# Kernel tuning notes

Measured on AMD Instinct MI355X. Metric: run time of the kernel, lower is better.

The kernel has to match this reference:

```python
import jax, jax.numpy as jnp
import numpy as np

N_NODES = 100000
N_EDGES = 3200000
N_GRAPHS = 128
HIDDEN = 128
DEPTH = 3


def setup_inputs() -> dict:
    key = jax.random.key(0)
    ks = jax.random.split(key, 12)
    x = jax.random.normal(ks[0], (N_NODES, 1), dtype=jnp.float32)
    edge_index = jax.random.randint(ks[1], (2, N_EDGES), 0, N_NODES, dtype=jnp.int64)
    batch = jnp.sort(jax.random.randint(ks[2], (N_NODES,), 0, N_GRAPHS, dtype=jnp.int64))
    s = 1.0 / np.sqrt(HIDDEN)
    return {
        "x": x,
        "edge_index": edge_index,
        "batch": batch,
        "W_emb": jax.random.normal(ks[3], (1, HIDDEN), dtype=jnp.float32),
        "b_emb": jax.random.normal(ks[4], (HIDDEN,), dtype=jnp.float32) * 0.01,
        "W_gnn": jax.random.normal(ks[5], (DEPTH, HIDDEN, HIDDEN), dtype=jnp.float32) * s,
        "b_gnn": jax.random.normal(ks[6], (DEPTH, HIDDEN), dtype=jnp.float32) * 0.01,
        "W_c1": jax.random.normal(ks[7], (HIDDEN, HIDDEN // 2), dtype=jnp.float32) * s,
        "b_c1": jax.random.normal(ks[8], (HIDDEN // 2,), dtype=jnp.float32) * 0.01,
        "W_c2": jax.random.normal(ks[9], (HIDDEN // 2, 1), dtype=jnp.float32) * s,
        "b_c2": jax.random.normal(ks[10], (1,), dtype=jnp.float32) * 0.01,
    }


def reference(x, edge_index, batch, W_emb, b_emb, W_gnn, b_gnn, W_c1, b_c1, W_c2, b_c2):
    # --- GCN normalization (self-loops + symmetric deg^-1/2) ---
    loop = jnp.arange(N_NODES, dtype=edge_index.dtype)
    row = jnp.concatenate([edge_index[0], loop])  # source nodes
    col = jnp.concatenate([edge_index[1], loop])  # target nodes
    deg = jax.ops.segment_sum(jnp.ones_like(col, dtype=jnp.float32), col, num_segments=N_NODES)
    dinv = jnp.where(deg > 0, jax.lax.rsqrt(jnp.maximum(deg, 1.0)), 0.0)
    norm = dinv[row] * dinv[col]  # [E+N]

    # --- node embedding ---
    h = x @ W_emb + b_emb  # [N, H]

    # --- GCN layers: linear -> gather -> normalize -> scatter-add -> bias -> relu ---
    for l in range(DEPTH):
        h_lin = h @ W_gnn[l]                       # [N, H]
        msgs = h_lin[row] * norm[:, None]          # [E+N, H]
        agg = jax.ops.segment_sum(msgs, col, num_segments=N_NODES)
        h = jax.nn.relu(agg + b_gnn[l])

    # --- global mean pool per graph ---
    counts = jax.ops.segment_sum(jnp.ones((N_NODES,), jnp.float32), batch, num_segments=N_GRAPHS)
    sums = jax.ops.segment_sum(h, batch, num_segments=N_GRAPHS)
    g = sums / jnp.maximum(counts, 1.0)[:, None]   # [G, H]

    # --- classifier (dropout is identity in eval) ---
    z = jax.nn.relu(g @ W_c1 + b_c1)
    out = jax.nn.sigmoid(z @ W_c2 + b_c2)          # [G, 1]
    return out.squeeze(-1)                          # [G]
```

## Files before the change

kernel.cpp:

```cpp
#include <hip/hip_runtime.h>
#include <math.h>

#define HID 128
#define CAP 96
#define TILE 8192
#define WSH 9
#define BUKCAP 24576

typedef unsigned int uint;
typedef unsigned short ushort;
typedef float f32x2 __attribute__((ext_vector_type(2)));
typedef float f32x4 __attribute__((ext_vector_type(4)));
typedef short bf16x8 __attribute__((ext_vector_type(8)));

__device__ inline ushort f2bf(float f) {
    uint u = __float_as_uint(f);
    return (ushort)((u + 0x7fffu + ((u >> 16) & 1u)) >> 16);
}
__device__ inline uint packbf(float a, float b) {
    return (uint)f2bf(a) | ((uint)f2bf(b) << 16);
}

__device__ inline f32x2 fp8lo(uint q) { return __builtin_amdgcn_cvt_pk_f32_fp8(q, false); }
__device__ inline f32x2 fp8hi(uint q) { return __builtin_amdgcn_cvt_pk_f32_fp8(q, true); }
__device__ inline uint pack4fp8(float a, float b, float c, float d) {
    int t = __builtin_amdgcn_cvt_pk_fp8_f32(a, b, 0, false);
    return (uint)__builtin_amdgcn_cvt_pk_fp8_f32(c, d, t, true);
}
__device__ inline long long as_i64(uint2 u) {
    union { uint2 a; long long b; } c;
    c.a = u;
    return c.b;
}


__global__ void __launch_bounds__(256) k_part(const int* __restrict__ row,
                                              const int* __restrict__ col,
                                              int* __restrict__ bukCur,
                                              uint* __restrict__ recs, int E) {
    __shared__ int hist[256];
    __shared__ int hist2[256];
    __shared__ uint base[256];
    int t = threadIdx.x;
    hist[t] = 0;
    hist2[t] = 0;
    __syncthreads();
    int i0 = blockIdx.x * TILE;
    int i1 = min(E, i0 + TILE);
    for (int i = i0 + t; i < i1; i += 256) {
        int b = col[i] >> WSH;
        atomicAdd(&hist[b], 1);
    }
    __syncthreads();
    if (hist[t] > 0) base[t] = (uint)atomicAdd(&bukCur[t], hist[t]);
    __syncthreads();
    for (int i = i0 + t; i < i1; i += 256) {
        int c = col[i];
        int b = c >> WSH;
        uint p = (uint)atomicAdd(&hist2[b], 1);
        uint idx = base[b] + p;
        if (idx < BUKCAP)
            recs[(size_t)b * BUKCAP + idx] = (uint)row[i] | ((uint)(c & 511) << 17);
    }
}

__global__ void __launch_bounds__(256) k_fbin(const uint* __restrict__ recs,
                                              const int* __restrict__ bukCur,
                                              const float* __restrict__ x,
                                              int* __restrict__ cnt,
                                              int* __restrict__ ebin,
                                              float* __restrict__ dinv,
                                              float2* __restrict__ pk0, int N) {
    __shared__ int lcnt[512];
    int b = blockIdx.x;
    int t = threadIdx.x;
    lcnt[t] = 0;
    lcnt[t + 256] = 0;
    __syncthreads();
    int n = min(bukCur[b], BUKCAP);
    const uint* rp = recs + (size_t)b * BUKCAP;
    int cbase = b << WSH;
    for (int j = t; j < n; j += 256) {
        uint u = rp[j];
        int r = (int)(u & 0x1FFFFu);
        int cl = (int)(u >> 17);
        int p = atomicAdd(&lcnt[cl], 1);
        if (p < CAP) ebin[(size_t)(cbase + cl) * CAP + p] = r << 5;
    }
    __syncthreads();
    int c0 = cbase + t;
    if (c0 < N) {
        cnt[c0] = lcnt[t];
        float d = rsqrtf((float)lcnt[t] + 1.0f);
        dinv[c0] = d;
        pk0[c0] = make_float2(d, d * x[c0]);
    }
    int c1 = cbase + t + 256;
    if (c1 < N) {
        cnt[c1] = lcnt[t + 256];
        float d = rsqrtf((float)lcnt[t + 256] + 1.0f);
        dinv[c1] = d;
        pk0[c1] = make_float2(d, d * x[c1]);
    }
}


__global__ void k_wprep(const float* __restrict__ W_emb, const float* __restrict__ b_emb,
                        const float* __restrict__ W_gnn,
                        float* __restrict__ u, float* __restrict__ v,
                        uint2* __restrict__ wfrag) {
    int b = blockIdx.x;
    int t = threadIdx.x;
    if (b < 16) {
        int gid = b * 256 + t;
        int l = gid >> 11;
        int rem = gid & 2047;
        int kb = rem >> 9;
        int nt = (rem >> 6) & 7;
        int lane = rem & 63;
        int k0 = kb * 32 + (lane >> 4) * 8;
        int n = nt * 16 + (lane & 15);
        const float* Wp = W_gnn + (size_t)(l + 1) * HID * HID;
        uint2 o;
        o.x = pack4fp8(Wp[(k0 + 0) * HID + n], Wp[(k0 + 1) * HID + n],
                       Wp[(k0 + 2) * HID + n], Wp[(k0 + 3) * HID + n]);
        o.y = pack4fp8(Wp[(k0 + 4) * HID + n], Wp[(k0 + 5) * HID + n],
                       Wp[(k0 + 6) * HID + n], Wp[(k0 + 7) * HID + n]);
        wfrag[gid] = o;
    } else if (t < HID) {
        float su = 0.f, sv = 0.f;
        for (int k = 0; k < HID; ++k) {
            float w = W_gnn[k * HID + t];
            su = fmaf(W_emb[k], w, su);
            sv = fmaf(b_emb[k], w, sv);
        }
        u[t] = su;
        v[t] = sv;
    }
}


__global__ void __launch_bounds__(256) k_sagg(const int* __restrict__ cnt,
                                              const int* __restrict__ ebin,
                                              const float* __restrict__ x,
                                              const float* __restrict__ dinv,
                                              const float2* __restrict__ pk0,
                                              const float* __restrict__ u,
                                              const float* __restrict__ v,
                                              const float* __restrict__ b0,
                                              uint* __restrict__ g8, int N) {
    __shared__ float sS0[256], sS1[256], sDc[256];
    int t = threadIdx.x;
    int c0 = blockIdx.x * 256;
    int c = c0 + t;
    if (c < N) {
        float dc = dinv[c];
        float A = 0.f, B = 0.f;
        int n = min(cnt[c], CAP);
        const int* bp = ebin + (size_t)c * CAP;
        int k = 0;
        for (; k + 4 <= n; k += 4) {
            float2 p0 = pk0[bp[k] >> 5], p1 = pk0[bp[k + 1] >> 5];
            float2 p2 = pk0[bp[k + 2] >> 5], p3 = pk0[bp[k + 3] >> 5];
            A += (p0.x + p1.x) + (p2.x + p3.x);
            B += (p0.y + p1.y) + (p2.y + p3.y);
        }
        for (; k < n; ++k) {
            float2 p = pk0[bp[k] >> 5];
            A += p.x;
            B += p.y;
        }
        float d2 = dc * dc;
        sS0[t] = fmaf(dc, A, d2);
        sS1[t] = fmaf(dc, B, d2 * x[c]);
        sDc[t] = dc;
    }
    __syncthreads();
    int nloc = min(256, N - c0);
    int total = nloc * 32;
    for (int gid = t; gid < total; gid += 256) {
        int lc = gid >> 5;
        int j = (gid & 31) * 4;
        float t1 = sS1[lc], t0 = sS0[lc], dc = sDc[lc];
        float v0 = fmaxf(fmaf(t1, u[j + 0], fmaf(t0, v[j + 0], b0[j + 0])), 0.f);
        float v1 = fmaxf(fmaf(t1, u[j + 1], fmaf(t0, v[j + 1], b0[j + 1])), 0.f);
        float v2 = fmaxf(fmaf(t1, u[j + 2], fmaf(t0, v[j + 2], b0[j + 2])), 0.f);
        float v3 = fmaxf(fmaf(t1, u[j + 3], fmaf(t0, v[j + 3], b0[j + 3])), 0.f);
        g8[(size_t)(c0 + lc) * 32 + (gid & 31)] = pack4fp8(dc * v0, dc * v1, dc * v2, dc * v3);
    }
}


__global__ void __launch_bounds__(256) k_agg(const int* __restrict__ cnt,
                                             const int* __restrict__ ebin,
                                             const float* __restrict__ dinv,
                                             const uint* __restrict__ g8,
                                             uint* __restrict__ a, int N) {
    int wave = (blockIdx.x * 256 + threadIdx.x) >> 6;
    if (wave >= N) return;
    int lane = threadIdx.x & 63;
    int c = wave;
    int ql = lane & 15;
    int qg = lane >> 4;
    const uint* __restrict__ gq = g8 + ql * 2;

    f32x2 a0 = {0.f, 0.f}, a1 = {0.f, 0.f}, a2 = {0.f, 0.f}, a3 = {0.f, 0.f};

    int n = min(cnt[c], CAP);
    int total = n + 1;
    const int* __restrict__ bp = ebin + (size_t)c * CAP - 1;

    for (int base = 0; base < total; base += 64) {
        int cw = min(total - base, 64);
        int gi = base + lane;
        int ro = 0;
        if (lane < cw) ro = (gi == 0) ? (c << 5) : bp[gi];
        int j = 0;
        for (; j + 16 <= cw; j += 16) {
            int o0 = __shfl(ro, j + qg);
            int o1 = __shfl(ro, j + 4 + qg);
            int o2 = __shfl(ro, j + 8 + qg);
            int o3 = __shfl(ro, j + 12 + qg);
            uint2 q0 = *(const uint2*)(gq + o0);
            uint2 q1 = *(const uint2*)(gq + o1);
            uint2 q2 = *(const uint2*)(gq + o2);
            uint2 q3 = *(const uint2*)(gq + o3);
            a0 += fp8lo(q0.x); a1 += fp8hi(q0.x); a2 += fp8lo(q0.y); a3 += fp8hi(q0.y);
            a0 += fp8lo(q1.x); a1 += fp8hi(q1.x); a2 += fp8lo(q1.y); a3 += fp8hi(q1.y);
            a0 += fp8lo(q2.x); a1 += fp8hi(q2.x); a2 += fp8lo(q2.y); a3 += fp8hi(q2.y);
            a0 += fp8lo(q3.x); a1 += fp8hi(q3.x); a2 += fp8lo(q3.y); a3 += fp8hi(q3.y);
        }
        for (; j + 4 <= cw; j += 4) {
            int o0 = __shfl(ro, j + qg);
            uint2 q0 = *(const uint2*)(gq + o0);
            a0 += fp8lo(q0.x); a1 += fp8hi(q0.x); a2 += fp8lo(q0.y); a3 += fp8hi(q0.y);
        }
        if (j < cw) {
            int e = j + qg;
            int o0 = __shfl(ro, min(e, cw - 1));
            uint2 q0 = *(const uint2*)(gq + o0);
            if (e >= cw) { q0.x = 0u; q0.y = 0u; }
            a0 += fp8lo(q0.x); a1 += fp8hi(q0.x); a2 += fp8lo(q0.y); a3 += fp8hi(q0.y);
        }
    }

    float r0 = a0.x, r1 = a0.y, r2 = a1.x, r3 = a1.y;
    float r4 = a2.x, r5 = a2.y, r6 = a3.x, r7 = a3.y;
#pragma unroll
    for (int m = 16; m <= 32; m <<= 1) {
        r0 += __shfl_xor(r0, m); r1 += __shfl_xor(r1, m);
        r2 += __shfl_xor(r2, m); r3 += __shfl_xor(r3, m);
        r4 += __shfl_xor(r4, m); r5 += __shfl_xor(r5, m);
        r6 += __shfl_xor(r6, m); r7 += __shfl_xor(r7, m);
    }
    if (qg == 0) {
        float dc = dinv[c];
        uint2 o;
        o.x = pack4fp8(dc * r0, dc * r1, dc * r2, dc * r3);
        o.y = pack4fp8(dc * r4, dc * r5, dc * r6, dc * r7);
        ((uint2*)(a + (size_t)c * 32))[ql] = o;
    }
}


#define RCH 32
__global__ void __launch_bounds__(256, 2) k_gemm(const uint* __restrict__ A,
                                                 const uint2* __restrict__ wfrag,
                                                 const float* __restrict__ bias,
                                                 const float* __restrict__ rowscale,
                                                 uint* __restrict__ H8, int N) {
    __shared__ uint2 sAf[4][2][64];
    __shared__ float sEp[4][16][68];
    int t = threadIdx.x;
    int w = t >> 6;
    int lane = t & 63;
    int rowgrp = w >> 1;
    int colh = w & 1;

    uint2 Bf[4][4];
#pragma unroll
    for (int kb = 0; kb < 4; ++kb)
#pragma unroll
        for (int i = 0; i < 4; ++i)
            Bf[kb][i] = wfrag[(kb * 8 + colh * 4 + i) * 64 + lane];

    float4 bb = ((const float4*)bias)[colh * 16 + (lane & 15)];

    int nchunk = (N + RCH - 1) / RCH;
    for (int ch = blockIdx.x; ch < nchunk; ch += gridDim.x) {
        int r0 = ch * RCH;
        __syncthreads();
        {
            int i = t;
#pragma unroll
            for (int s = 0; s < 2; ++s, i += 256) {
                int kb = i >> 7;
                int rg = (i >> 6) & 1;
                int ln = i & 63;
                int gr = r0 + rg * 16 + (ln & 15);
                gr = min(gr, N - 1);
                sAf[kb][rg][ln] = ((const uint2*)(A + (size_t)gr * 32))[kb * 4 + (ln >> 4)];
            }
        }
        __syncthreads();

        f32x4 acc[4] = {{0.f, 0.f, 0.f, 0.f}, {0.f, 0.f, 0.f, 0.f},
                        {0.f, 0.f, 0.f, 0.f}, {0.f, 0.f, 0.f, 0.f}};
#pragma unroll
        for (int kb = 0; kb < 4; ++kb) {
            long long af = as_i64(sAf[kb][rowgrp][lane]);
#pragma unroll
            for (int i = 0; i < 4; ++i)
                acc[i] = __builtin_amdgcn_mfma_f32_16x16x32_fp8_fp8(af, as_i64(Bf[kb][i]),
                                                                    acc[i], 0, 0, 0);
        }

#pragma unroll
        for (int i = 0; i < 4; ++i) {
#pragma unroll
            for (int reg = 0; reg < 4; ++reg)
                sEp[w][(lane >> 4) * 4 + reg][i * 16 + (lane & 15)] = acc[i][reg];
        }
#pragma unroll
        for (int e = 0; e < 4; ++e) {
            int rr = (lane >> 4) + 4 * e;
            int cu = lane & 15;
            const float* sp = &sEp[w][rr][cu * 4];
            int rowg = r0 + rowgrp * 16 + rr;
            if (rowg < N) {
                float sc = rowscale ? rowscale[rowg] : 1.0f;
                float o0 = sc * fmaxf(sp[0] + bb.x, 0.f);
                float o1 = sc * fmaxf(sp[1] + bb.y, 0.f);
                float o2 = sc * fmaxf(sp[2] + bb.z, 0.f);
                float o3 = sc * fmaxf(sp[3] + bb.w, 0.f);
                H8[(size_t)rowg * 32 + colh * 16 + cu] = pack4fp8(o0, o1, o2, o3);
            }
        }
    }
}


__global__ void k_pool(const uint* __restrict__ h8, const int* __restrict__ batch,
                       float* __restrict__ gpool, float* __restrict__ gcnt, int N) {
    int gi = blockIdx.x >> 2, part = blockIdx.x & 3;
    int t = threadIdx.x;
    int ui = t & 31;
    int sub = t >> 5;
    int lo = 0, hi = N;
    while (lo < hi) { int m = (lo + hi) >> 1; if (batch[m] < gi) lo = m + 1; else hi = m; }
    int start = lo;
    lo = start; hi = N;
    while (lo < hi) { int m = (lo + hi) >> 1; if (batch[m] <= gi) lo = m + 1; else hi = m; }
    int end = lo;
    if (part == 0 && t == 0) gcnt[gi] = (float)(end - start);
    int len = end - start;
    int q = (len + 15) >> 4;
    int seg = part * 4 + sub;
    int rs = start + seg * q;
    int re = min(end, rs + q);
    float s0 = 0.f, s1 = 0.f, s2 = 0.f, s3 = 0.f;
    for (int i = rs; i < re; ++i) {
        uint qq = h8[(size_t)i * 32 + ui];
        f32x2 lo2 = fp8lo(qq), hi2 = fp8hi(qq);
        s0 += lo2.x; s1 += lo2.y; s2 += hi2.x; s3 += hi2.y;
    }
    if (re > rs) {
        float* gp = gpool + gi * HID + ui * 4;
        atomicAdd(gp + 0, s0);
        atomicAdd(gp + 1, s1);
        atomicAdd(gp + 2, s2);
        atomicAdd(gp + 3, s3);
    }
}

__global__ void k_cls(const float* __restrict__ gpool, const float* __restrict__ gcnt,
                      const float* __restrict__ Wc1, const float* __restrict__ bc1,
                      const float* __restrict__ Wc2, const float* __restrict__ bc2,
                      float* __restrict__ out) {
    int g = blockIdx.x;
    int j = threadIdx.x;
    float inv = 1.0f / fmaxf(gcnt[g], 1.0f);
    float z = bc1[j];
    for (int k = 0; k < HID; ++k) z = fmaf(gpool[g * HID + k] * inv, Wc1[k * 64 + j], z);
    z = fmaxf(z, 0.f);
    float p = z * Wc2[j];
    for (int off = 32; off; off >>= 1) p += __shfl_down(p, off);
    if (j == 0) out[g] = 1.0f / (1.0f + expf(-(p + bc2[0])));
}


extern "C" void kernel_launch(void* const* d_in, const int* in_sizes, int n_in,
                              void* d_out, int out_size, void* d_ws, size_t ws_size,
                              hipStream_t stream) {
    const float* x     = (const float*)d_in[0];
    const int*   eidx  = (const int*)d_in[1];
    const int*   batch = (const int*)d_in[2];
    const float* W_emb = (const float*)d_in[3];
    const float* b_emb = (const float*)d_in[4];
    const float* W_gnn = (const float*)d_in[5];
    const float* b_gnn = (const float*)d_in[6];
    const float* W_c1  = (const float*)d_in[7];
    const float* b_c1  = (const float*)d_in[8];
    const float* W_c2  = (const float*)d_in[9];
    const float* b_c2  = (const float*)d_in[10];

    const int N = in_sizes[0];
    const int E = in_sizes[1] / 2;
    const int G = out_size;
    const int* row = eidx;
    const int* col = eidx + E;
    const int NBUK = (N + 511) >> WSH;

    char* ws = (char*)d_ws;
    auto alloc = [&](size_t bytes) -> void* {
        void* p = (void*)ws;
        ws += (bytes + 255) & ~(size_t)255;
        return p;
    };
    int*    cnt    = (int*)alloc((size_t)N * 4);
    float*  dinv   = (float*)alloc((size_t)N * 4);
    float2* pk0    = (float2*)alloc((size_t)N * 8);
    int*    bukCur = (int*)alloc(256 * 4);
    uint*   recs   = (uint*)alloc((size_t)NBUK * BUKCAP * 4);
    int*    ebin   = (int*)alloc((size_t)N * CAP * 4);
    float*  u      = (float*)alloc(HID * 4);
    float*  v      = (float*)alloc(HID * 4);
    uint*   G8     = (uint*)alloc((size_t)N * 32 * 4);
    uint*   A      = (uint*)alloc((size_t)N * 32 * 4);
    uint2*  wfrag  = (uint2*)alloc(4096 * 8);
    float*  gpool  = (float*)alloc((size_t)G * HID * 4);
    float*  gcnt   = (float*)alloc((size_t)G * 4);

    hipMemsetAsync(bukCur, 0, 256 * 4, stream);
    hipMemsetAsync(gpool, 0, (size_t)G * HID * 4, stream);

    k_part<<<(E + TILE - 1) / TILE, 256, 0, stream>>>(row, col, bukCur, recs, E);
    k_fbin<<<NBUK, 256, 0, stream>>>(recs, bukCur, x, cnt, ebin, dinv, pk0, N);

    k_wprep<<<17, 256, 0, stream>>>(W_emb, b_emb, W_gnn, u, v, wfrag);

    k_sagg<<<(N + 255) / 256, 256, 0, stream>>>(cnt, ebin, x, dinv, pk0, u, v, b_gnn, G8, N);

    int nchunk = (N + RCH - 1) / RCH;
    int gblk = nchunk < 768 ? nchunk : 768;
    for (int l = 1; l < 3; ++l) {
        k_agg<<<(N + 3) / 4, 256, 0, stream>>>(cnt, ebin, dinv, G8, A, N);
        k_gemm<<<gblk, 256, 0, stream>>>(A, wfrag + (size_t)(l - 1) * 2048,
                                         b_gnn + (size_t)l * HID,
                                         (l == 1) ? dinv : (const float*)nullptr,
                                         G8, N);
    }

    k_pool<<<G * 4, 128, 0, stream>>>(G8, batch, gpool, gcnt, N);
    k_cls<<<G, 64, 0, stream>>>(gpool, gcnt, W_c1, b_c1, W_c2, b_c2, (float*)d_out);
}
```

Baseline: 372.8 us.

## Fuse neighbor aggregation with fp8 MFMA GEMM into one per-layer kernel

Merges the separate aggregation kernel and the GEMM kernel into one kernel. Each block gathers 32 destination rows, writes the aggregated fp8 rows straight into the shared-memory A-fragment layout, then runs the MFMA GEMM and epilogue. The aim is to drop the intermediate A buffer round trip through global memory and one launch per layer, so the output now ping-pongs between two buffers. In exchange, each wave handles 8 rows serially with launch bounds set for 2 blocks, which may cut the latency hiding of the gather and add per-block weight-fragment loads.

After: 433.3 us. 16.2% more time.

```diff
diff --git a/kernel.cpp b/kernel.cpp
--- a/kernel.cpp
+++ b/kernel.cpp
@@ -191,89 +191,21 @@
 }
 
 
-__global__ void __launch_bounds__(256) k_agg(const int* __restrict__ cnt,
-                                             const int* __restrict__ ebin,
-                                             const float* __restrict__ dinv,
-                                             const uint* __restrict__ g8,
-                                             uint* __restrict__ a, int N) {
-    int wave = (blockIdx.x * 256 + threadIdx.x) >> 6;
-    if (wave >= N) return;
-    int lane = threadIdx.x & 63;
-    int c = wave;
+__global__ void __launch_bounds__(256, 2) k_fag(const int* __restrict__ cnt,
+                                                const int* __restrict__ ebin,
+                                                const float* __restrict__ dinv,
+                                                const uint* __restrict__ g8in,
+                                                const uint2* __restrict__ wfrag,
+                                                const float* __restrict__ bias,
+                                                const float* __restrict__ rowscale,
+                                                uint* __restrict__ g8out, int N) {
+    __shared__ uint2 sAf[4][2][64];
+    __shared__ float sEp[4][16][68];
+    int t = threadIdx.x;
+    int w = t >> 6;
+    int lane = t & 63;
     int ql = lane & 15;
     int qg = lane >> 4;
-    const uint* __restrict__ gq = g8 + ql * 2;
-
-    f32x2 a0 = {0.f, 0.f}, a1 = {0.f, 0.f}, a2 = {0.f, 0.f}, a3 = {0.f, 0.f};
-
-    int n = min(cnt[c], CAP);
-    int total = n + 1;
-    const int* __restrict__ bp = ebin + (size_t)c * CAP - 1;
-
-    for (int base = 0; base < total; base += 64) {
-        int cw = min(total - base, 64);
-        int gi = base + lane;
-        int ro = 0;
-        if (lane < cw) ro = (gi == 0) ? (c << 5) : bp[gi];
-        int j = 0;
-        for (; j + 16 <= cw; j += 16) {
-            int o0 = __shfl(ro, j + qg);
-            int o1 = __shfl(ro, j + 4 + qg);
-            int o2 = __shfl(ro, j + 8 + qg);
-            int o3 = __shfl(ro, j + 12 + qg);
-            uint2 q0 = *(const uint2*)(gq + o0);
-            uint2 q1 = *(const uint2*)(gq + o1);
-            uint2 q2 = *(const uint2*)(gq + o2);
-            uint2 q3 = *(const uint2*)(gq + o3);
-            a0 += fp8lo(q0.x); a1 += fp8hi(q0.x); a2 += fp8lo(q0.y); a3 += fp8hi(q0.y);
-            a0 += fp8lo(q1.x); a1 += fp8hi(q1.x); a2 += fp8lo(q1.y); a3 += fp8hi(q1.y);
-            a0 += fp8lo(q2.x); a1 += fp8hi(q2.x); a2 += fp8lo(q2.y); a3 += fp8hi(q2.y);
-            a0 += fp8lo(q3.x); a1 += fp8hi(q3.x); a2 += fp8lo(q3.y); a3 += fp8hi(q3.y);
-        }
-        for (; j + 4 <= cw; j += 4) {
-            int o0 = __shfl(ro, j + qg);
-            uint2 q0 = *(const uint2*)(gq + o0);
-            a0 += fp8lo(q0.x); a1 += fp8hi(q0.x); a2 += fp8lo(q0.y); a3 += fp8hi(q0.y);
-        }
-        if (j < cw) {
-            int e = j + qg;
-            int o0 = __shfl(ro, min(e, cw - 1));
-            uint2 q0 = *(const uint2*)(gq + o0);
-            if (e >= cw) { q0.x = 0u; q0.y = 0u; }
-            a0 += fp8lo(q0.x); a1 += fp8hi(q0.x); a2 += fp8lo(q0.y); a3 += fp8hi(q0.y);
-        }
-    }
-
-    float r0 = a0.x, r1 = a0.y, r2 = a1.x, r3 = a1.y;
-    float r4 = a2.x, r5 = a2.y, r6 = a3.x, r7 = a3.y;
-#pragma unroll
-    for (int m = 16; m <= 32; m <<= 1) {
-        r0 += __shfl_xor(r0, m); r1 += __shfl_xor(r1, m);
-        r2 += __shfl_xor(r2, m); r3 += __shfl_xor(r3, m);
-        r4 += __shfl_xor(r4, m); r5 += __shfl_xor(r5, m);
-        r6 += __shfl_xor(r6, m); r7 += __shfl_xor(r7, m);
-    }
-    if (qg == 0) {
-        float dc = dinv[c];
-        uint2 o;
-        o.x = pack4fp8(dc * r0, dc * r1, dc * r2, dc * r3);
-        o.y = pack4fp8(dc * r4, dc * r5, dc * r6, dc * r7);
-        ((uint2*)(a + (size_t)c * 32))[ql] = o;
-    }
-}
-
-
-#define RCH 32
-__global__ void __launch_bounds__(256, 2) k_gemm(const uint* __restrict__ A,
-                                                 const uint2* __restrict__ wfrag,
-                                                 const float* __restrict__ bias,
-                                                 const float* __restrict__ rowscale,
-                                                 uint* __restrict__ H8, int N) {
-    __shared__ uint2 sAf[4][2][64];
-    __shared__ float sEp[4][16][68];
-    int t = threadIdx.x;
-    int w = t >> 6;
-    int lane = t & 63;
     int rowgrp = w >> 1;
     int colh = w & 1;
 
@@ -283,58 +215,103 @@
 #pragma unroll
         for (int i = 0; i < 4; ++i)
             Bf[kb][i] = wfrag[(kb * 8 + colh * 4 + i) * 64 + lane];
-
     float4 bb = ((const float4*)bias)[colh * 16 + (lane & 15)];
 
-    int nchunk = (N + RCH - 1) / RCH;
-    for (int ch = blockIdx.x; ch < nchunk; ch += gridDim.x) {
-        int r0 = ch * RCH;
-        __syncthreads();
-        {
-            int i = t;
-#pragma unroll
-            for (int s = 0; s < 2; ++s, i += 256) {
-                int kb = i >> 7;
-                int rg = (i >> 6) & 1;
-                int ln = i & 63;
-                int gr = r0 + rg * 16 + (ln & 15);
-                gr = min(gr, N - 1);
-                sAf[kb][rg][ln] = ((const uint2*)(A + (size_t)gr * 32))[kb * 4 + (ln >> 4)];
+    int rbase = blockIdx.x * 32;
+    const uint* __restrict__ gq = g8in + ql * 2;
+
+    for (int i = 0; i < 8; ++i) {
+        int lr = (w << 3) + i;
+        int c = min(rbase + lr, N - 1);
+
+        f32x2 a0 = {0.f, 0.f}, a1 = {0.f, 0.f}, a2 = {0.f, 0.f}, a3 = {0.f, 0.f};
+        int n = min(cnt[c], CAP);
+        int total = n + 1;
+        const int* __restrict__ bp = ebin + (size_t)c * CAP - 1;
+
+        for (int base = 0; base < total; base += 64) {
+            int cw = min(total - base, 64);
+            int gi = base + lane;
+            int ro = 0;
+            if (lane < cw) ro = (gi == 0) ? (c << 5) : bp[gi];
+            int j = 0;
+            for (; j + 16 <= cw; j += 16) {
+                int o0 = __shfl(ro, j + qg);
+                int o1 = __shfl(ro, j + 4 + qg);
+                int o2 = __shfl(ro, j + 8 + qg);
+                int o3 = __shfl(ro, j + 12 + qg);
+                uint2 q0 = *(const uint2*)(gq + o0);
+                uint2 q1 = *(const uint2*)(gq + o1);
+                uint2 q2 = *(const uint2*)(gq + o2);
+                uint2 q3 = *(const uint2*)(gq + o3);
+                a0 += fp8lo(q0.x); a1 += fp8hi(q0.x); a2 += fp8lo(q0.y); a3 += fp8hi(q0.y);
+                a0 += fp8lo(q1.x); a1 += fp8hi(q1.x); a2 += fp8lo(q1.y); a3 += fp8hi(q1.y);
+                a0 += fp8lo(q2.x); a1 += fp8hi(q2.x); a2 += fp8lo(q2.y); a3 += fp8hi(q2.y);
+                a0 += fp8lo(q3.x); a1 += fp8hi(q3.x); a2 += fp8lo(q3.y); a3 += fp8hi(q3.y);
             }
-        }
-        __syncthreads();
-
-        f32x4 acc[4] = {{0.f, 0.f, 0.f, 0.f}, {0.f, 0.f, 0.f, 0.f},
-                        {0.f, 0.f, 0.f, 0.f}, {0.f, 0.f, 0.f, 0.f}};
-#pragma unroll
-        for (int kb = 0; kb < 4; ++kb) {
-            long long af = as_i64(sAf[kb][rowgrp][lane]);
-#pragma unroll
-            for (int i = 0; i < 4; ++i)
-                acc[i] = __builtin_amdgcn_mfma_f32_16x16x32_fp8_fp8(af, as_i64(Bf[kb][i]),
-                                                                    acc[i], 0, 0, 0);
-        }
-
-#pragma unroll
-        for (int i = 0; i < 4; ++i) {
-#pragma unroll
-            for (int reg = 0; reg < 4; ++reg)
-                sEp[w][(lane >> 4) * 4 + reg][i * 16 + (lane & 15)] = acc[i][reg];
-        }
-#pragma unroll
-        for (int e = 0; e < 4; ++e) {
-            int rr = (lane >> 4) + 4 * e;
-            int cu = lane & 15;
-            const float* sp = &sEp[w][rr][cu * 4];
-            int rowg = r0 + rowgrp * 16 + rr;
-            if (rowg < N) {
-                float sc = rowscale ? rowscale[rowg] : 1.0f;
-                float o0 = sc * fmaxf(sp[0] + bb.x, 0.f);
-                float o1 = sc * fmaxf(sp[1] + bb.y, 0.f);
-                float o2 = sc * fmaxf(sp[2] + bb.z, 0.f);
-                float o3 = sc * fmaxf(sp[3] + bb.w, 0.f);
-                H8[(size_t)rowg * 32 + colh * 16 + cu] = pack4fp8(o0, o1, o2, o3);
+            for (; j + 4 <= cw; j += 4) {
+                int o0 = __shfl(ro, j + qg);
+                uint2 q0 = *(const uint2*)(gq + o0);
+                a0 += fp8lo(q0.x); a1 += fp8hi(q0.x); a2 += fp8lo(q0.y); a3 += fp8hi(q0.y);
             }
+            if (j < cw) {
+                int e = j + qg;
+                int o0 = __shfl(ro, min(e, cw - 1));
+                uint2 q0 = *(const uint2*)(gq + o0);
+                if (e >= cw) { q0.x = 0u; q0.y = 0u; }
+                a0 += fp8lo(q0.x); a1 += fp8hi(q0.x); a2 += fp8lo(q0.y); a3 += fp8hi(q0.y);
+            }
+        }
+
+        float s0 = a0.x, s1 = a0.y, s2 = a1.x, s3 = a1.y;
+        float s4 = a2.x, s5 = a2.y, s6 = a3.x, s7 = a3.y;
+#pragma unroll
+        for (int m = 16; m <= 32; m <<= 1) {
+            s0 += __shfl_xor(s0, m); s1 += __shfl_xor(s1, m);
+            s2 += __shfl_xor(s2, m); s3 += __shfl_xor(s3, m);
+            s4 += __shfl_xor(s4, m); s5 += __shfl_xor(s5, m);
+            s6 += __shfl_xor(s6, m); s7 += __shfl_xor(s7, m);
+        }
+        if (qg == 0) {
+            float dc = dinv[c];
+            uint2 o;
+            o.x = pack4fp8(dc * s0, dc * s1, dc * s2, dc * s3);
+            o.y = pack4fp8(dc * s4, dc * s5, dc * s6, dc * s7);
+            sAf[ql >> 2][lr >> 4][((ql & 3) << 4) | (lr & 15)] = o;
+        }
+    }
+    __syncthreads();
+
+    f32x4 acc[4] = {{0.f, 0.f, 0.f, 0.f}, {0.f, 0.f, 0.f, 0.f},
+                    {0.f, 0.f, 0.f, 0.f}, {0.f, 0.f, 0.f, 0.f}};
+#pragma unroll
+    for (int kb = 0; kb < 4; ++kb) {
+        long long af = as_i64(sAf[kb][rowgrp][lane]);
+#pragma unroll
+        for (int i = 0; i < 4; ++i)
+            acc[i] = __builtin_amdgcn_mfma_f32_16x16x32_fp8_fp8(af, as_i64(Bf[kb][i]),
+                                                                acc[i], 0, 0, 0);
+    }
+
+#pragma unroll
+    for (int i = 0; i < 4; ++i) {
+#pragma unroll
+        for (int reg = 0; reg < 4; ++reg)
+            sEp[w][(lane >> 4) * 4 + reg][i * 16 + (lane & 15)] = acc[i][reg];
+    }
+#pragma unroll
+    for (int e = 0; e < 4; ++e) {
+        int rr = (lane >> 4) + 4 * e;
+        int cu = lane & 15;
+        const float* sp = &sEp[w][rr][cu * 4];
+        int rowg = rbase + rowgrp * 16 + rr;
+        if (rowg < N) {
+            float sc = rowscale ? rowscale[rowg] : 1.0f;
+            float o0 = sc * fmaxf(sp[0] + bb.x, 0.f);
+            float o1 = sc * fmaxf(sp[1] + bb.y, 0.f);
+            float o2 = sc * fmaxf(sp[2] + bb.z, 0.f);
+            float o3 = sc * fmaxf(sp[3] + bb.w, 0.f);
+            g8out[(size_t)rowg * 32 + colh * 16 + cu] = pack4fp8(o0, o1, o2, o3);
         }
     }
 }
@@ -425,8 +402,8 @@
     int*    ebin   = (int*)alloc((size_t)N * CAP * 4);
     float*  u      = (float*)alloc(HID * 4);
     float*  v      = (float*)alloc(HID * 4);
-    uint*   G8     = (uint*)alloc((size_t)N * 32 * 4);
-    uint*   A      = (uint*)alloc((size_t)N * 32 * 4);
+    uint*   G8a    = (uint*)alloc((size_t)N * 32 * 4);
+    uint*   G8b    = (uint*)alloc((size_t)N * 32 * 4);
     uint2*  wfrag  = (uint2*)alloc(4096 * 8);
     float*  gpool  = (float*)alloc((size_t)G * HID * 4);
     float*  gcnt   = (float*)alloc((size_t)G * 4);
@@ -439,18 +416,19 @@
 
     k_wprep<<<17, 256, 0, stream>>>(W_emb, b_emb, W_gnn, u, v, wfrag);
 
-    k_sagg<<<(N + 255) / 256, 256, 0, stream>>>(cnt, ebin, x, dinv, pk0, u, v, b_gnn, G8, N);
-
-    int nchunk = (N + RCH - 1) / RCH;
-    int gblk = nchunk < 768 ? nchunk : 768;
+    k_sagg<<<(N + 255) / 256, 256, 0, stream>>>(cnt, ebin, x, dinv, pk0, u, v, b_gnn, G8a, N);
+
+    uint* bin = G8a;
+    uint* bout = G8b;
     for (int l = 1; l < 3; ++l) {
-        k_agg<<<(N + 3) / 4, 256, 0, stream>>>(cnt, ebin, dinv, G8, A, N);
-        k_gemm<<<gblk, 256, 0, stream>>>(A, wfrag + (size_t)(l - 1) * 2048,
-                                         b_gnn + (size_t)l * HID,
-                                         (l == 1) ? dinv : (const float*)nullptr,
-                                         G8, N);
-    }
-
-    k_pool<<<G * 4, 128, 0, stream>>>(G8, batch, gpool, gcnt, N);
+        k_fag<<<(N + 31) / 32, 256, 0, stream>>>(cnt, ebin, dinv, bin,
+                                                 wfrag + (size_t)(l - 1) * 2048,
+                                                 b_gnn + (size_t)l * HID,
+                                                 (l == 1) ? dinv : (const float*)nullptr,
+                                                 bout, N);
+        uint* tmp = bin; bin = bout; bout = tmp;
+    }
+
+    k_pool<<<G * 4, 128, 0, stream>>>(bin, batch, gpool, gcnt, N);
     k_cls<<<G, 64, 0, stream>>>(gpool, gcnt, W_c1, b_c1, W_c2, b_c2, (float*)d_out);
 }
```

## Split fbin buckets across four blocks and use 16 lanes per node in sagg

Applied to the files above, without the earlier changes.

k_fbin now launches four blocks per bucket, each handling a 128-column quarter selected from the record's high bits. Every block still scans the whole bucket but only processes matching records. k_sagg changes from one thread per node to 16 lanes per node with a shuffle reduction, so the per-edge gathers spread across more threads and lanes read adjacent edge-list entries. The cost is that each fbin block rereads the full bucket (four times the record traffic), and sagg now runs many more small blocks.

Measured after the change: 361.2 us. -3.1%, faster.

```diff
diff --git a/kernel.cpp b/kernel.cpp
--- a/kernel.cpp
+++ b/kernel.cpp
@@ -71,36 +71,33 @@
                                               int* __restrict__ ebin,
                                               float* __restrict__ dinv,
                                               float2* __restrict__ pk0, int N) {
-    __shared__ int lcnt[512];
-    int b = blockIdx.x;
-    int t = threadIdx.x;
-    lcnt[t] = 0;
-    lcnt[t + 256] = 0;
+    __shared__ int lcnt[128];
+    int b = blockIdx.x >> 2;
+    int q = blockIdx.x & 3;
+    int t = threadIdx.x;
+    if (t < 128) lcnt[t] = 0;
     __syncthreads();
     int n = min(bukCur[b], BUKCAP);
     const uint* rp = recs + (size_t)b * BUKCAP;
-    int cbase = b << WSH;
+    int cbase = (b << WSH) + (q << 7);
     for (int j = t; j < n; j += 256) {
         uint u = rp[j];
-        int r = (int)(u & 0x1FFFFu);
-        int cl = (int)(u >> 17);
-        int p = atomicAdd(&lcnt[cl], 1);
-        if (p < CAP) ebin[(size_t)(cbase + cl) * CAP + p] = r << 5;
-    }
-    __syncthreads();
-    int c0 = cbase + t;
-    if (c0 < N) {
-        cnt[c0] = lcnt[t];
-        float d = rsqrtf((float)lcnt[t] + 1.0f);
-        dinv[c0] = d;
-        pk0[c0] = make_float2(d, d * x[c0]);
-    }
-    int c1 = cbase + t + 256;
-    if (c1 < N) {
-        cnt[c1] = lcnt[t + 256];
-        float d = rsqrtf((float)lcnt[t + 256] + 1.0f);
-        dinv[c1] = d;
-        pk0[c1] = make_float2(d, d * x[c1]);
+        if ((int)(u >> 24) == q) {
+            int r = (int)(u & 0x1FFFFu);
+            int cl = (int)((u >> 17) & 127u);
+            int p = atomicAdd(&lcnt[cl], 1);
+            if (p < CAP) ebin[(size_t)(cbase + cl) * CAP + p] = r << 5;
+        }
+    }
+    __syncthreads();
+    if (t < 128) {
+        int c = cbase + t;
+        if (c < N) {
+            cnt[c] = lcnt[t];
+            float d = rsqrtf((float)lcnt[t] + 1.0f);
+            dinv[c] = d;
+            pk0[c] = make_float2(d, d * x[c]);
+        }
     }
 }
 
@@ -149,44 +146,54 @@
                                               const float* __restrict__ v,
                                               const float* __restrict__ b0,
                                               uint* __restrict__ g8, int N) {
-    __shared__ float sS0[256], sS1[256], sDc[256];
-    int t = threadIdx.x;
-    int c0 = blockIdx.x * 256;
-    int c = c0 + t;
+    __shared__ float sS0[16], sS1[16], sDc[16];
+    int t = threadIdx.x;
+    int qw = t >> 4;
+    int ll = t & 15;
+    int c0 = blockIdx.x * 16;
+    int c = c0 + qw;
+    float A = 0.f, B = 0.f;
+    float dc = 0.f;
     if (c < N) {
-        float dc = dinv[c];
-        float A = 0.f, B = 0.f;
+        dc = dinv[c];
         int n = min(cnt[c], CAP);
         const int* bp = ebin + (size_t)c * CAP;
-        int k = 0;
-        for (; k + 4 <= n; k += 4) {
-            float2 p0 = pk0[bp[k] >> 5], p1 = pk0[bp[k + 1] >> 5];
-            float2 p2 = pk0[bp[k + 2] >> 5], p3 = pk0[bp[k + 3] >> 5];
-            A += (p0.x + p1.x) + (p2.x + p3.x);
-            B += (p0.y + p1.y) + (p2.y + p3.y);
-        }
-        for (; k < n; ++k) {
+        int k = ll;
+        for (; k + 16 < n; k += 32) {
+            int o0 = bp[k], o1 = bp[k + 16];
+            float2 p0 = pk0[o0 >> 5], p1 = pk0[o1 >> 5];
+            A += p0.x + p1.x;
+            B += p0.y + p1.y;
+        }
+        if (k < n) {
             float2 p = pk0[bp[k] >> 5];
             A += p.x;
             B += p.y;
         }
+    }
+#pragma unroll
+    for (int m = 1; m <= 8; m <<= 1) {
+        A += __shfl_xor(A, m);
+        B += __shfl_xor(B, m);
+    }
+    if (ll == 0 && c < N) {
         float d2 = dc * dc;
-        sS0[t] = fmaf(dc, A, d2);
-        sS1[t] = fmaf(dc, B, d2 * x[c]);
-        sDc[t] = dc;
-    }
-    __syncthreads();
-    int nloc = min(256, N - c0);
+        sS0[qw] = fmaf(dc, A, d2);
+        sS1[qw] = fmaf(dc, B, d2 * x[c]);
+        sDc[qw] = dc;
+    }
+    __syncthreads();
+    int nloc = min(16, N - c0);
     int total = nloc * 32;
     for (int gid = t; gid < total; gid += 256) {
         int lc = gid >> 5;
         int j = (gid & 31) * 4;
-        float t1 = sS1[lc], t0 = sS0[lc], dc = sDc[lc];
+        float t1 = sS1[lc], t0 = sS0[lc], dcc = sDc[lc];
         float v0 = fmaxf(fmaf(t1, u[j + 0], fmaf(t0, v[j + 0], b0[j + 0])), 0.f);
         float v1 = fmaxf(fmaf(t1, u[j + 1], fmaf(t0, v[j + 1], b0[j + 1])), 0.f);
         float v2 = fmaxf(fmaf(t1, u[j + 2], fmaf(t0, v[j + 2], b0[j + 2])), 0.f);
         float v3 = fmaxf(fmaf(t1, u[j + 3], fmaf(t0, v[j + 3], b0[j + 3])), 0.f);
-        g8[(size_t)(c0 + lc) * 32 + (gid & 31)] = pack4fp8(dc * v0, dc * v1, dc * v2, dc * v3);
+        g8[(size_t)(c0 + lc) * 32 + (gid & 31)] = pack4fp8(dcc * v0, dcc * v1, dcc * v2, dcc * v3);
     }
 }
 
@@ -435,11 +442,11 @@
     hipMemsetAsync(gpool, 0, (size_t)G * HID * 4, stream);
 
     k_part<<<(E + TILE - 1) / TILE, 256, 0, stream>>>(row, col, bukCur, recs, E);
-    k_fbin<<<NBUK, 256, 0, stream>>>(recs, bukCur, x, cnt, ebin, dinv, pk0, N);
+    k_fbin<<<NBUK * 4, 256, 0, stream>>>(recs, bukCur, x, cnt, ebin, dinv, pk0, N);
 
     k_wprep<<<17, 256, 0, stream>>>(W_emb, b_emb, W_gnn, u, v, wfrag);
 
-    k_sagg<<<(N + 255) / 256, 256, 0, stream>>>(cnt, ebin, x, dinv, pk0, u, v, b_gnn, G8, N);
+    k_sagg<<<(N + 15) / 16, 256, 0, stream>>>(cnt, ebin, x, dinv, pk0, u, v, b_gnn, G8, N);
 
     int nchunk = (N + RCH - 1) / RCH;
     int gblk = nchunk < 768 ? nchunk : 768;
```
